# Kernel tuning notes

Hardware: AMD Instinct MI355X
Metric: run time of the kernel (lower is better)

The kernel has to match this reference:

```python
import jax, jax.numpy as jnp
import numpy as np

H = 12        # attention heads
BETA = 0.5    # blend weight between ctx-cosine probs and QK probs
LN_EPS = 1e-12


def layer_norm(x, g, b):
    mu = x.mean(-1, keepdims=True)
    var = ((x - mu) ** 2).mean(-1, keepdims=True)
    return (x - mu) * jax.lax.rsqrt(var + LN_EPS) * g + b


def setup_inputs() -> dict:
    key = jax.random.key(0)
    B, S, D, F, L = 16, 512, 768, 3072, 4
    ks = jax.random.split(key, 9)
    w = lambda k, shape: (jax.random.normal(k, shape, jnp.float32) * 0.02)
    return {
        "hidden_states": jax.random.normal(ks[0], (B, S, D), jnp.float32),
        "Wq": w(ks[1], (L, D, D)), "bq": jnp.zeros((L, D), jnp.float32),
        "Wk": w(ks[2], (L, D, D)), "bk": jnp.zeros((L, D), jnp.float32),
        "Wv": w(ks[3], (L, D, D)), "bv": jnp.zeros((L, D), jnp.float32),
        "Wc": w(ks[4], (L, D, D)), "bc": jnp.zeros((L, D), jnp.float32),
        "Wo": w(ks[5], (L, D, D)), "bo": jnp.zeros((L, D), jnp.float32),
        "g1": jnp.ones((L, D), jnp.float32), "b1": jnp.zeros((L, D), jnp.float32),
        "Wi": w(ks[6], (L, D, F)), "bi": jnp.zeros((L, F), jnp.float32),
        "Wo2": w(ks[7], (L, F, D)), "bo2": jnp.zeros((L, D), jnp.float32),
        "g2": jnp.ones((L, D), jnp.float32), "b2": jnp.zeros((L, D), jnp.float32),
    }


def reference(hidden_states, Wq, bq, Wk, bk, Wv, bv, Wc, bc, Wo, bo,
              g1, b1, Wi, bi, Wo2, bo2, g2, b2):
    B, S, D = hidden_states.shape
    Dh = D // H
    L = Wq.shape[0]
    eye = jnp.eye(S, dtype=hidden_states.dtype)
    scale = 1.0 / np.sqrt(Dh).astype(np.float32)

    def heads(t):  # [B,S,D] -> [B,H,S,Dh]
        return t.reshape(B, S, H, Dh).transpose(0, 2, 1, 3)

    x = hidden_states
    for i in range(L):  # small fixed layer loop
        q = heads(x @ Wq[i] + bq[i])
        k = heads(x @ Wk[i] + bk[i])
        v = heads(x @ Wv[i] + bv[i])
        c = heads(x @ Wc[i] + bc[i])

        # Branch 1: cosine-normalized context scores, flipped (1 - cos) + I
        cn = jnp.linalg.norm(c, axis=-1, keepdims=True)           # [B,H,S,1]
        denom = cn * jnp.swapaxes(cn, -1, -2)                     # [B,H,S,S]
        s1 = 1.0 - jnp.einsum('bhld,bhrd->bhlr', c, c) / denom + eye
        p1 = jax.nn.softmax(s1, axis=-1)

        # Branch 2: standard scaled QK scores
        s2 = jnp.einsum('bhld,bhrd->bhlr', q, k) * scale
        p2 = jax.nn.softmax(s2, axis=-1)

        p = BETA * p1 + (1.0 - BETA) * p2                          # beta blend
        ctx = jnp.einsum('bhlr,bhrd->bhld', p, v)                  # [B,H,S,Dh]
        ctx = ctx.transpose(0, 2, 1, 3).reshape(B, S, D)

        attn_out = layer_norm(ctx @ Wo[i] + bo[i] + x, g1[i], b1[i])
        h = jax.nn.gelu(attn_out @ Wi[i] + bi[i], approximate=False)
        x = layer_norm(h @ Wo2[i] + bo2[i] + attn_out, g2[i], b2[i])
    return x
```

## Files before the change

kernel.cpp:

```cpp
#include <hip/hip_runtime.h>
#include <math.h>

#define DD 768
#define FF 3072
#define SS 512
#define BB 16
#define NH 12
#define DH 64
#define NL 4
#define MM (BB*SS)

typedef __attribute__((ext_vector_type(8))) short short8;
typedef __attribute__((ext_vector_type(4))) float f32x4;

__device__ __forceinline__ unsigned short f2bf(float f) {
  unsigned u = __float_as_uint(f);
  return (unsigned short)((u + 0x7FFFu + ((u >> 16) & 1u)) >> 16);
}
__device__ __forceinline__ float bf2f(unsigned short s) {
  return __uint_as_float(((unsigned)s) << 16);
}

#define GLOAD_LDS(g, l) \
  __builtin_amdgcn_global_load_lds((const __attribute__((address_space(1))) void*)(g), \
                                   (__attribute__((address_space(3))) void*)(l), 16, 0, 0)

__global__ __launch_bounds__(256) void cvt_dual_k(const float* __restrict__ in,
                                                  float* __restrict__ outf,
                                                  unsigned short* __restrict__ outb, int n) {
  for (int i = blockIdx.x*256 + threadIdx.x; i < n; i += gridDim.x*256) {
    float v = in[i]; outf[i] = v; outb[i] = f2bf(v);
  }
}

__global__ __launch_bounds__(256) void tcvt_k(const float* __restrict__ src,
                                              unsigned short* __restrict__ dst,
                                              int K, int N) {
  __shared__ float t[32][33];
  const int n0 = blockIdx.x*32, k0 = blockIdx.y*32;
  const int tx = threadIdx.x & 31, ty = threadIdx.x >> 5;
#pragma unroll
  for (int i = 0; i < 32; i += 8)
    t[ty+i][tx] = src[(size_t)(k0+ty+i)*N + n0+tx];
  __syncthreads();
#pragma unroll
  for (int i = 0; i < 32; i += 8)
    dst[(size_t)(n0+ty+i)*K + k0+tx] = f2bf(t[tx][ty+i]);
}

__global__ __launch_bounds__(256) void bcat_k(const float* __restrict__ a,
                                              const float* __restrict__ b,
                                              const float* __restrict__ c,
                                              const float* __restrict__ d,
                                              float* __restrict__ out) {
  int i = blockIdx.x*256 + threadIdx.x;
  int w = i / 768;
  const float* s = (w == 0) ? a : (w == 1) ? b : (w == 2) ? c : d;
  out[i] = s[i - w*768];
}

template<int EPI, int OBF>
__global__ __launch_bounds__(256, 3) void mgemm_k(
    const unsigned short* __restrict__ A,
    const unsigned short* __restrict__ Bw,
    const float* __restrict__ bias,
    const float* __restrict__ resid,
    void* __restrict__ Cout, int M, int N, int K)
{
  __shared__ __align__(16) unsigned short As[2][128*32];
  __shared__ __align__(16) unsigned short Bs[2][128*32];
  const int nwg = gridDim.x * gridDim.y;
  int lin = blockIdx.y * gridDim.x + blockIdx.x;
  lin = (lin & 7) * (nwg >> 3) + (lin >> 3);
  const int bm = (lin / gridDim.x) * 128, bn = (lin % gridDim.x) * 128;
  const int tid = threadIdx.x;
  const int wave = tid >> 6, lane = tid & 63;
  const int wm = (wave >> 1)*64, wn = (wave & 1)*64;
  const int woff = wave*32*32;

  f32x4 acc[4][4] = {};

  const unsigned short* Ag = A  + (size_t)(bm + wave*32 + (lane>>2))*K + (lane&3)*8;
  const unsigned short* Bg = Bw + (size_t)(bn + wave*32 + (lane>>2))*K + (lane&3)*8;

  GLOAD_LDS(Ag,                As[0] + woff);
  GLOAD_LDS(Ag + 16*(size_t)K, As[0] + woff + 16*32);
  GLOAD_LDS(Bg,                Bs[0] + woff);
  GLOAD_LDS(Bg + 16*(size_t)K, Bs[0] + woff + 16*32);
  Ag += 32; Bg += 32;
  __syncthreads();

  const unsigned short* Ac = As[0]; unsigned short* An = As[1];
  const unsigned short* Bc = Bs[0]; unsigned short* Bn = Bs[1];
  const int nk = K >> 5;

#pragma unroll 1
  for (int t = 0; t < nk - 1; ++t) {
    GLOAD_LDS(Ag,                An + woff);
    GLOAD_LDS(Ag + 16*(size_t)K, An + woff + 16*32);
    GLOAD_LDS(Bg,                Bn + woff);
    GLOAD_LDS(Bg + 16*(size_t)K, Bn + woff + 16*32);
    Ag += 32; Bg += 32;

    short8 af[4], bfr[4];
#pragma unroll
    for (int i = 0; i < 4; ++i) {
      af[i]  = *(const short8*)&Ac[(wm + i*16 + (lane & 15))*32 + (lane >> 4)*8];
      bfr[i] = *(const short8*)&Bc[(wn + i*16 + (lane & 15))*32 + (lane >> 4)*8];
    }
    __builtin_amdgcn_s_setprio(1);
#pragma unroll
    for (int i = 0; i < 4; ++i)
#pragma unroll
      for (int j = 0; j < 4; ++j)
        acc[i][j] = __builtin_amdgcn_mfma_f32_16x16x32_bf16(af[i], bfr[j], acc[i][j], 0, 0, 0);
    __builtin_amdgcn_s_setprio(0);

    __syncthreads();
    const unsigned short* tA = Ac; Ac = An; An = (unsigned short*)tA;
    const unsigned short* tB = Bc; Bc = Bn; Bn = (unsigned short*)tB;
  }

  {
    short8 af[4], bfr[4];
#pragma unroll
    for (int i = 0; i < 4; ++i) {
      af[i]  = *(const short8*)&Ac[(wm + i*16 + (lane & 15))*32 + (lane >> 4)*8];
      bfr[i] = *(const short8*)&Bc[(wn + i*16 + (lane & 15))*32 + (lane >> 4)*8];
    }
#pragma unroll
    for (int i = 0; i < 4; ++i)
#pragma unroll
      for (int j = 0; j < 4; ++j)
        acc[i][j] = __builtin_amdgcn_mfma_f32_16x16x32_bf16(af[i], bfr[j], acc[i][j], 0, 0, 0);
  }

  const int col0 = bn + wn + (lane & 15);
  const int row0 = bm + wm + (lane >> 4)*4;
#pragma unroll
  for (int i = 0; i < 4; ++i) {
#pragma unroll
    for (int j = 0; j < 4; ++j) {
      const int n = col0 + j*16;
      const float bv = bias[n];
#pragma unroll
      for (int r = 0; r < 4; ++r) {
        const int m = row0 + i*16 + r;
        float v = acc[i][j][r] + bv;
        if (EPI == 1) v += resid[(size_t)m*N + n];
        if (EPI == 2) v = 0.5f*v*(1.0f + erff(v*0.70710678118654752f));
        if (OBF) ((unsigned short*)Cout)[(size_t)m*N + n] = f2bf(v);
        else     ((float*)Cout)[(size_t)m*N + n] = v;
      }
    }
  }
}

__global__ __launch_bounds__(256) void cnorm_k(const unsigned short* __restrict__ c,
                                               float* __restrict__ rn) {
  int idx = blockIdx.x*4 + (threadIdx.x >> 6);
  int lane = threadIdx.x & 63;
  int s  = idx % SS;
  int bh = idx / SS;
  int h  = bh % NH;
  int b  = bh / NH;
  float v = bf2f(c[((size_t)(b*SS + s))*FF + h*DH + lane]);
  float ss = v*v;
#pragma unroll
  for (int off = 32; off; off >>= 1) ss += __shfl_xor(ss, off, 64);
  if (lane == 0) rn[idx] = rsqrtf(ss);
}

__global__ __launch_bounds__(256) void vtrans_k(const unsigned short* __restrict__ v,
                                                unsigned short* __restrict__ VT) {
  __shared__ unsigned short t[64][72];
  const int s0 = blockIdx.x*64;
  const int h  = blockIdx.y;
  const int b  = blockIdx.z;
  const size_t base = (size_t)(b*SS)*FF + h*DH;
  const int row = threadIdx.x >> 2, seg = threadIdx.x & 3;
  const unsigned short* vg = v + base + (size_t)(s0+row)*FF + seg*16;
  *(uint4*)&t[row][seg*16]     = *(const uint4*)vg;
  *(uint4*)&t[row][seg*16 + 8] = *(const uint4*)(vg + 8);
  __syncthreads();
  unsigned short o[16];
#pragma unroll
  for (int u = 0; u < 16; ++u) o[u] = t[seg*16 + u][row];
  unsigned short* og = VT + ((size_t)(b*NH + h)*DH + row)*SS + s0 + seg*16;
  *(uint4*)og       = *(const uint4*)&o[0];
  *(uint4*)(og + 8) = *(const uint4*)&o[8];
}

__global__ __launch_bounds__(256, 3) void attn5_k(
    const unsigned short* __restrict__ q, const unsigned short* __restrict__ k,
    const unsigned short* __restrict__ c, const float* __restrict__ rn,
    const unsigned short* __restrict__ VT, unsigned short* __restrict__ ctxO)
{
  const int bid = blockIdx.x + 8*blockIdx.y + 96*blockIdx.z;
  const int l0  = ((bid >> 3) & 7) << 6;
  const int bh  = (bid & 7) + ((bid >> 6) << 3);
  const int h   = bh % NH;
  const int b   = bh / NH;
  const int tid = threadIdx.x;
  const int wave = tid >> 6, lane = tid & 63;
  const int wm = wave * 16;
  const int fr = lane & 15;
  const int fg = lane >> 4;
  const size_t base   = (size_t)(b*SS)*FF + h*DH;
  const size_t vtbase = (size_t)bh*DH*SS;

  __shared__ __align__(16) unsigned short Ks [2][64*72];
  __shared__ __align__(16) unsigned short Crs[2][64*72];
  __shared__ __align__(16) unsigned short Ps [4][16*72];
  unsigned short* Pw = Ps[wave];

  const unsigned short* qrow = q + base + (size_t)(l0 + wm + fr)*FF + fg*8;
  const unsigned short* crow = c + base + (size_t)(l0 + wm + fr)*FF + fg*8;
  const short8 aQ0 = *(const short8*)qrow;
  const short8 aQ1 = *(const short8*)(qrow + 32);
  const short8 aC0 = *(const short8*)crow;
  const short8 aC1 = *(const short8*)(crow + 32);

  float rnl[4];
#pragma unroll
  for (int reg = 0; reg < 4; ++reg)
    rnl[reg] = rn[(size_t)bh*SS + l0 + wm + fg*4 + reg];

  const int srow = tid >> 2, sseg = tid & 3;
  {
    const unsigned short* kg = k + base + (size_t)srow*FF + sseg*16;
    const unsigned short* cg = c + base + (size_t)srow*FF + sseg*16;
    *(uint4*)&Ks [0][srow*72 + sseg*16]     = *(const uint4*)kg;
    *(uint4*)&Ks [0][srow*72 + sseg*16 + 8] = *(const uint4*)(kg + 8);
    *(uint4*)&Crs[0][srow*72 + sseg*16]     = *(const uint4*)cg;
    *(uint4*)&Crs[0][srow*72 + sseg*16 + 8] = *(const uint4*)(cg + 8);
  }
  __syncthreads();

  float rs2[4], rs1[4];
#pragma unroll
  for (int r = 0; r < 4; ++r) { rs2[r] = 0.f; rs1[r] = 0.f; }
  f32x4 oc1[4] = {}, oc2[4] = {};

#pragma unroll 1
  for (int it = 0; it < 8; ++it) {
    const int r0 = it*64;
    const int cur = it & 1, nxt = cur ^ 1;

    uint4 nk0, nk1, nc0, nc1;
    if (it < 7) {
      const unsigned short* kg = k + base + (size_t)(r0 + 64 + srow)*FF + sseg*16;
      const unsigned short* cg = c + base + (size_t)(r0 + 64 + srow)*FF + sseg*16;
      nk0 = *(const uint4*)kg;  nk1 = *(const uint4*)(kg + 8);
      nc0 = *(const uint4*)cg;  nc1 = *(const uint4*)(cg + 8);
    }

    float rnr[4];
    short8 bv0[4], bv1[4];
#pragma unroll
    for (int nt = 0; nt < 4; ++nt) {
      rnr[nt] = rn[(size_t)bh*SS + r0 + nt*16 + fr];
      const unsigned short* vtr = VT + vtbase + (size_t)(nt*16 + fr)*SS + r0 + fg*8;
      bv0[nt] = *(const short8*)vtr;
      bv1[nt] = *(const short8*)(vtr + 32);
    }

    f32x4 s1a[4] = {}, s2a[4] = {};
#pragma unroll
    for (int nt = 0; nt < 4; ++nt) {
      const short8 bK0 = *(const short8*)&Ks [cur][(nt*16+fr)*72 + fg*8];
      const short8 bK1 = *(const short8*)&Ks [cur][(nt*16+fr)*72 + fg*8 + 32];
      const short8 bC0 = *(const short8*)&Crs[cur][(nt*16+fr)*72 + fg*8];
      const short8 bC1 = *(const short8*)&Crs[cur][(nt*16+fr)*72 + fg*8 + 32];
      s2a[nt] = __builtin_amdgcn_mfma_f32_16x16x32_bf16(aQ0, bK0, s2a[nt], 0,0,0);
      s2a[nt] = __builtin_amdgcn_mfma_f32_16x16x32_bf16(aQ1, bK1, s2a[nt], 0,0,0);
      s1a[nt] = __builtin_amdgcn_mfma_f32_16x16x32_bf16(aC0, bC0, s1a[nt], 0,0,0);
      s1a[nt] = __builtin_amdgcn_mfma_f32_16x16x32_bf16(aC1, bC1, s1a[nt], 0,0,0);
    }

    float sv1[4][4], sv2[4][4];
#pragma unroll
    for (int nt = 0; nt < 4; ++nt)
#pragma unroll
      for (int reg = 0; reg < 4; ++reg) {
        const int ql = wm + fg*4 + reg;
        const int rr = nt*16 + fr;
        sv2[reg][nt] = s2a[nt][reg] * 0.125f;
        sv1[reg][nt] = 1.0f - s1a[nt][reg]*rnl[reg]*rnr[nt]
                     + ((l0+ql) == (r0+rr) ? 1.0f : 0.0f);
      }

#pragma unroll
    for (int reg = 0; reg < 4; ++reg) {
      const int prow = (fg*4 + reg)*72;
#pragma unroll
      for (int nt = 0; nt < 4; ++nt) {
        const float x1 = __expf(sv1[reg][nt] - 3.0f);
        Pw[prow + nt*16 + fr] = f2bf(x1);
        rs1[reg] += x1;
      }
    }
    {
      const short8 p0 = *(const short8*)&Pw[fr*72 + fg*8];
      const short8 p1 = *(const short8*)&Pw[fr*72 + fg*8 + 32];
#pragma unroll
      for (int nt = 0; nt < 4; ++nt) {
        oc1[nt] = __builtin_amdgcn_mfma_f32_16x16x32_bf16(p0, bv0[nt], oc1[nt], 0,0,0);
        oc1[nt] = __builtin_amdgcn_mfma_f32_16x16x32_bf16(p1, bv1[nt], oc1[nt], 0,0,0);
      }
    }

#pragma unroll
    for (int reg = 0; reg < 4; ++reg) {
      const int prow = (fg*4 + reg)*72;
#pragma unroll
      for (int nt = 0; nt < 4; ++nt) {
        const float x2 = __expf(sv2[reg][nt] - 3.0f);
        Pw[prow + nt*16 + fr] = f2bf(x2);
        rs2[reg] += x2;
      }
    }
    {
      const short8 p0 = *(const short8*)&Pw[fr*72 + fg*8];
      const short8 p1 = *(const short8*)&Pw[fr*72 + fg*8 + 32];
#pragma unroll
      for (int nt = 0; nt < 4; ++nt) {
        oc2[nt] = __builtin_amdgcn_mfma_f32_16x16x32_bf16(p0, bv0[nt], oc2[nt], 0,0,0);
        oc2[nt] = __builtin_amdgcn_mfma_f32_16x16x32_bf16(p1, bv1[nt], oc2[nt], 0,0,0);
      }
    }

    if (it < 7) {
      *(uint4*)&Ks [nxt][srow*72 + sseg*16]     = nk0;
      *(uint4*)&Ks [nxt][srow*72 + sseg*16 + 8] = nk1;
      *(uint4*)&Crs[nxt][srow*72 + sseg*16]     = nc0;
      *(uint4*)&Crs[nxt][srow*72 + sseg*16 + 8] = nc1;
    }
    __syncthreads();
  }

#pragma unroll
  for (int reg = 0; reg < 4; ++reg) {
    float t1 = rs1[reg], t2 = rs2[reg];
#pragma unroll
    for (int off = 1; off < 16; off <<= 1) {
      t1 += __shfl_xor(t1, off, 64);
      t2 += __shfl_xor(t2, off, 64);
    }
    const float i1 = 0.5f / t1;
    const float i2 = 0.5f / t2;
    const int prow = (fg*4 + reg)*72;
#pragma unroll
    for (int nt = 0; nt < 4; ++nt)
      Pw[prow + nt*16 + fr] = f2bf(oc1[nt][reg]*i1 + oc2[nt][reg]*i2);
  }
  {
    const int row = lane >> 2, seg = lane & 3;
    const int Mrow = b*SS + l0 + wm + row;
    unsigned short* og = ctxO + (size_t)Mrow*DD + h*DH + seg*16;
    *(uint4*)og       = *(const uint4*)&Pw[row*72 + seg*16];
    *(uint4*)(og + 8) = *(const uint4*)&Pw[row*72 + seg*16 + 8];
  }
}

__global__ __launch_bounds__(256) void ln_k(const float* __restrict__ in,
                                            const float* __restrict__ g,
                                            const float* __restrict__ b,
                                            float* __restrict__ outf,
                                            unsigned short* __restrict__ outb) {
  __shared__ float xs[DD];
  __shared__ float red[4];
  const int tid = threadIdx.x;
  const float* xr = in + (size_t)blockIdx.x * DD;
  float* xo = outf + (size_t)blockIdx.x * DD;
  unsigned short* xbr = outb + (size_t)blockIdx.x * DD;
  float s = 0.f;
  for (int d = tid; d < DD; d += 256) { float v = xr[d]; xs[d] = v; s += v; }
#pragma unroll
  for (int off = 32; off; off >>= 1) s += __shfl_xor(s, off, 64);
  if ((tid & 63) == 0) red[tid >> 6] = s;
  __syncthreads();
  float mu = (red[0]+red[1]+red[2]+red[3]) * (1.f/DD);
  __syncthreads();
  float s2 = 0.f;
  for (int d = tid; d < DD; d += 256) { float t = xs[d]-mu; s2 += t*t; }
#pragma unroll
  for (int off = 32; off; off >>= 1) s2 += __shfl_xor(s2, off, 64);
  if ((tid & 63) == 0) red[tid >> 6] = s2;
  __syncthreads();
  float var = (red[0]+red[1]+red[2]+red[3]) * (1.f/DD);
  float rstd = rsqrtf(var + 1e-12f);
  for (int d = tid; d < DD; d += 256) {
    float o = (xs[d]-mu)*rstd*g[d] + b[d];
    xo[d] = o;
    xbr[d] = f2bf(o);
  }
}

extern "C" void kernel_launch(void* const* d_in, const int* in_sizes, int n_in,
                              void* d_out, int out_size, void* d_ws, size_t ws_size,
                              hipStream_t stream) {
  const float* hs  = (const float*)d_in[0];
  const float* Wq  = (const float*)d_in[1];  const float* bq  = (const float*)d_in[2];
  const float* Wk  = (const float*)d_in[3];  const float* bk  = (const float*)d_in[4];
  const float* Wv  = (const float*)d_in[5];  const float* bv  = (const float*)d_in[6];
  const float* Wc  = (const float*)d_in[7];  const float* bc  = (const float*)d_in[8];
  const float* Wo  = (const float*)d_in[9];  const float* bo  = (const float*)d_in[10];
  const float* g1  = (const float*)d_in[11]; const float* b1  = (const float*)d_in[12];
  const float* Wi  = (const float*)d_in[13]; const float* bi  = (const float*)d_in[14];
  const float* Wo2 = (const float*)d_in[15]; const float* bo2 = (const float*)d_in[16];
  const float* g2  = (const float*)d_in[17]; const float* b2  = (const float*)d_in[18];

  const size_t XN  = (size_t)MM * DD;
  const size_t HN  = (size_t)MM * FF;
  const int    nBH = BB*NH*SS;
  const size_t WTN = 7667712;

  char* p = (char*)d_ws;
  float*          x      = (float*)p;           p += XN*4;
  float*          attnf  = (float*)p;           p += XN*4;
  unsigned short* qkvc16 = (unsigned short*)p;  p += HN*2;
  unsigned short* xb16   = (unsigned short*)p;  p += XN*2;
  unsigned short* ctx16  = (unsigned short*)p;  p += XN*2;
  unsigned short* attn16 = (unsigned short*)p;  p += XN*2;
  unsigned short* vt16   = (unsigned short*)p;  p += XN*2;
  unsigned short* WT     = (unsigned short*)p;  p += WTN*2;
  float*          bqkvc  = (float*)p;           p += 3072*4;
  float*          cnb    = (float*)p;           p += (size_t)nBH*4;
  const size_t need = (size_t)(p - (char*)d_ws);
  if (ws_size < need) return;

  unsigned short* WqkvcT = WT;
  unsigned short* WoT    = WT + 2359296;
  unsigned short* WiT    = WT + 2949120;
  unsigned short* Wo2T   = WT + 5308416;
  unsigned short* hb16   = qkvc16;

  cvt_dual_k<<<4096, 256, 0, stream>>>(hs, x, xb16, (int)XN);

  dim3 gGQ(FF/128, MM/128);
  dim3 gGD(DD/128, MM/128);
  dim3 gA(SS/64, NH, BB);
  dim3 tDD(DD/32, DD/32);
  dim3 tDF(FF/32, DD/32);
  dim3 tFD(DD/32, FF/32);

  for (int i = 0; i < NL; ++i) {
    const size_t wD = (size_t)i*DD*DD, wF = (size_t)i*DD*FF;
    tcvt_k<<<tDD, 256, 0, stream>>>(Wq + wD, WqkvcT,            DD, DD);
    tcvt_k<<<tDD, 256, 0, stream>>>(Wk + wD, WqkvcT +  768*768, DD, DD);
    tcvt_k<<<tDD, 256, 0, stream>>>(Wv + wD, WqkvcT + 1536*768, DD, DD);
    tcvt_k<<<tDD, 256, 0, stream>>>(Wc + wD, WqkvcT + 2304*768, DD, DD);
    tcvt_k<<<tDD, 256, 0, stream>>>(Wo + wD, WoT,  DD, DD);
    tcvt_k<<<tDF, 256, 0, stream>>>(Wi + wF, WiT,  DD, FF);
    tcvt_k<<<tFD, 256, 0, stream>>>(Wo2 + wF, Wo2T, FF, DD);
    bcat_k<<<12, 256, 0, stream>>>(bq + (size_t)i*DD, bk + (size_t)i*DD,
                                   bv + (size_t)i*DD, bc + (size_t)i*DD, bqkvc);

    mgemm_k<0,1><<<gGQ, 256, 0, stream>>>(xb16, WqkvcT, bqkvc, nullptr, qkvc16, MM, FF, DD);

    cnorm_k<<<nBH/4, 256, 0, stream>>>(qkvc16 + 2304, cnb);
    vtrans_k<<<gA, 256, 0, stream>>>(qkvc16 + 1536, vt16);
    attn5_k<<<gA, 256, 0, stream>>>(qkvc16, qkvc16 + 768, qkvc16 + 2304,
                                    cnb, vt16, ctx16);

    mgemm_k<1,0><<<gGD, 256, 0, stream>>>(ctx16, WoT, bo + (size_t)i*DD, x, attnf, MM, DD, DD);
    ln_k<<<MM, 256, 0, stream>>>(attnf, g1 + (size_t)i*DD, b1 + (size_t)i*DD, attnf, attn16);

    mgemm_k<2,1><<<gGQ, 256, 0, stream>>>(attn16, WiT, bi + (size_t)i*FF, nullptr, hb16, MM, FF, DD);
    mgemm_k<1,0><<<gGD, 256, 0, stream>>>(hb16, Wo2T, bo2 + (size_t)i*DD, attnf, x, MM, DD, FF);
    float* lnout = (i == NL-1) ? (float*)d_out : x;
    ln_k<<<MM, 256, 0, stream>>>(x, g2 + (size_t)i*DD, b2 + (size_t)i*DD, lnout, xb16);
  }
}
```

Before: 1.474 ms.

## Add 256x256 tile GEMM kernel for QKVC and FFN-up projections

Adds a new 512-thread GEMM kernel with 256x256 output tiles, double-buffered LDS filled by direct global-to-LDS loads, XOR-swizzled reads, an interleaved load/MFMA schedule with priority hints, and a grid remap for locality. It replaces the 128x128 GEMM for the two N=3072 projections (fused QKVC and the GELU up-projection). The larger tiles raise operand reuse and cut global traffic, and the staged schedule overlaps loads with matrix math. In exchange it uses much more LDS and many more accumulator registers per block, and it launches only 384 workgroups, which may leave some compute units underused or unevenly loaded.

Measured after the change: 1.565 ms. 6.2% more time.

```diff
diff --git a/kernel.cpp b/kernel.cpp
--- a/kernel.cpp
+++ b/kernel.cpp
@@ -156,6 +156,143 @@
   }
 }
 
+template<int EPI>
+__global__ __launch_bounds__(512, 2) void mg256_k(
+    const unsigned short* __restrict__ A,
+    const unsigned short* __restrict__ Bw,
+    const float* __restrict__ bias,
+    unsigned short* __restrict__ Cout, int M, int N, int K)
+{
+  __shared__ __align__(16) unsigned short Ab[2][256*64];
+  __shared__ __align__(16) unsigned short Bb[2][256*64];
+  const int nwg = gridDim.x * gridDim.y;
+  int lin = blockIdx.y * gridDim.x + blockIdx.x;
+  lin = (lin & 7) * (nwg >> 3) + (lin >> 3);
+  const int bm = (lin / gridDim.x) * 256, bn = (lin % gridDim.x) * 256;
+  const int tid = threadIdx.x;
+  const int wave = tid >> 6, lane = tid & 63;
+  const int wr = wave >> 2, wc = wave & 3;
+  const int fr = lane & 15, fg = lane >> 4;
+  const int xsw = (fr & 8) ? 4 : 0;
+
+  f32x4 acc[8][4] = {};
+  short8 bfrag[4][2];
+
+  const int srow = tid >> 3;
+  const int sseg = (tid & 7) ^ ((wave & 1) << 2);
+  const unsigned short* Asrc = A  + (size_t)(bm + srow)*K + sseg*8;
+  const unsigned short* Bsrc = Bw + (size_t)(bn + srow)*K + sseg*8;
+  const int ldst = wave * 512;
+
+#define MG_STGA(q, bf, kk) GLOAD_LDS(Asrc + (size_t)((q)*64)*K + (kk), &Ab[bf][(q)*4096 + ldst])
+#define MG_STGB(q, bf, kk) GLOAD_LDS(Bsrc + (size_t)((q)*64)*K + (kk), &Bb[bf][(q)*4096 + ldst])
+
+  const int arow0 = wr*128 + fr;
+  const int brow0 = wc*64 + fr;
+#define MG_A(m, s) (*(const short8*)&Ac[(arow0 + (m)*16)*64 + ((((s)*4) + fg) ^ xsw)*8])
+#define MG_B(n, s) (*(const short8*)&Bc[(brow0 + (n)*16)*64 + ((((s)*4) + fg) ^ xsw)*8])
+
+#define MG_MFMA(m0, a00, a01, a10, a11) do { \
+    __builtin_amdgcn_s_setprio(1); \
+    _Pragma("unroll") \
+    for (int n = 0; n < 4; ++n) { \
+      acc[m0][n]   = __builtin_amdgcn_mfma_f32_16x16x32_bf16(a00, bfrag[n][0], acc[m0][n],   0,0,0); \
+      acc[m0][n]   = __builtin_amdgcn_mfma_f32_16x16x32_bf16(a01, bfrag[n][1], acc[m0][n],   0,0,0); \
+      acc[m0+1][n] = __builtin_amdgcn_mfma_f32_16x16x32_bf16(a10, bfrag[n][0], acc[m0+1][n], 0,0,0); \
+      acc[m0+1][n] = __builtin_amdgcn_mfma_f32_16x16x32_bf16(a11, bfrag[n][1], acc[m0+1][n], 0,0,0); \
+    } \
+    __builtin_amdgcn_s_setprio(0); } while (0)
+
+  const int nk = K >> 6;
+
+  MG_STGB(0, 0, 0); MG_STGB(1, 0, 0); MG_STGB(2, 0, 0); MG_STGB(3, 0, 0);
+  MG_STGA(0, 0, 0); MG_STGA(2, 0, 0); MG_STGA(1, 0, 0); MG_STGA(3, 0, 0);
+  asm volatile("s_waitcnt vmcnt(2)" ::: "memory");
+  __builtin_amdgcn_sched_barrier(0);
+  __builtin_amdgcn_s_barrier();
+
+  int cur = 0;
+#pragma unroll 1
+  for (int t = 0; t < nk - 1; ++t) {
+    const int nx = cur ^ 1;
+    const int kk = (t + 1) << 6;
+    const unsigned short* Ac = Ab[cur];
+    const unsigned short* Bc = Bb[cur];
+    short8 x0, x1, y0, y1;
+    x0 = MG_A(0,0); x1 = MG_A(0,1); y0 = MG_A(1,0); y1 = MG_A(1,1);
+#pragma unroll
+    for (int n = 0; n < 4; ++n) { bfrag[n][0] = MG_B(n,0); bfrag[n][1] = MG_B(n,1); }
+    MG_STGB(0, nx, kk); MG_STGB(1, nx, kk);
+    __builtin_amdgcn_s_barrier();
+    MG_MFMA(0, x0, x1, y0, y1);
+    __builtin_amdgcn_s_barrier();
+    x0 = MG_A(2,0); x1 = MG_A(2,1); y0 = MG_A(3,0); y1 = MG_A(3,1);
+    MG_STGB(2, nx, kk); MG_STGB(3, nx, kk);
+    __builtin_amdgcn_s_barrier();
+    MG_MFMA(2, x0, x1, y0, y1);
+    asm volatile("s_waitcnt vmcnt(4)" ::: "memory");
+    __builtin_amdgcn_sched_barrier(0);
+    __builtin_amdgcn_s_barrier();
+    x0 = MG_A(4,0); x1 = MG_A(4,1); y0 = MG_A(5,0); y1 = MG_A(5,1);
+    MG_STGA(0, nx, kk); MG_STGA(2, nx, kk);
+    __builtin_amdgcn_s_barrier();
+    MG_MFMA(4, x0, x1, y0, y1);
+    __builtin_amdgcn_s_barrier();
+    x0 = MG_A(6,0); x1 = MG_A(6,1); y0 = MG_A(7,0); y1 = MG_A(7,1);
+    MG_STGA(1, nx, kk); MG_STGA(3, nx, kk);
+    __builtin_amdgcn_s_barrier();
+    MG_MFMA(6, x0, x1, y0, y1);
+    asm volatile("s_waitcnt vmcnt(2)" ::: "memory");
+    __builtin_amdgcn_sched_barrier(0);
+    __builtin_amdgcn_s_barrier();
+    cur = nx;
+  }
+  {
+    const unsigned short* Ac = Ab[cur];
+    const unsigned short* Bc = Bb[cur];
+    short8 x0, x1, y0, y1;
+    x0 = MG_A(0,0); x1 = MG_A(0,1); y0 = MG_A(1,0); y1 = MG_A(1,1);
+#pragma unroll
+    for (int n = 0; n < 4; ++n) { bfrag[n][0] = MG_B(n,0); bfrag[n][1] = MG_B(n,1); }
+    __builtin_amdgcn_s_barrier();
+    MG_MFMA(0, x0, x1, y0, y1);
+    __builtin_amdgcn_s_barrier();
+    x0 = MG_A(2,0); x1 = MG_A(2,1); y0 = MG_A(3,0); y1 = MG_A(3,1);
+    __builtin_amdgcn_s_barrier();
+    MG_MFMA(2, x0, x1, y0, y1);
+    asm volatile("s_waitcnt vmcnt(0)" ::: "memory");
+    __builtin_amdgcn_sched_barrier(0);
+    __builtin_amdgcn_s_barrier();
+    x0 = MG_A(4,0); x1 = MG_A(4,1); y0 = MG_A(5,0); y1 = MG_A(5,1);
+    __builtin_amdgcn_s_barrier();
+    MG_MFMA(4, x0, x1, y0, y1);
+    __builtin_amdgcn_s_barrier();
+    x0 = MG_A(6,0); x1 = MG_A(6,1); y0 = MG_A(7,0); y1 = MG_A(7,1);
+    MG_MFMA(6, x0, x1, y0, y1);
+  }
+#undef MG_STGA
+#undef MG_STGB
+#undef MG_A
+#undef MG_B
+#undef MG_MFMA
+
+  const int crow0 = bm + wr*128 + fg*4;
+  const int ccol0 = bn + wc*64 + fr;
+#pragma unroll
+  for (int n = 0; n < 4; ++n) {
+    const float bv = bias[ccol0 + n*16];
+#pragma unroll
+    for (int m = 0; m < 8; ++m) {
+#pragma unroll
+      for (int r = 0; r < 4; ++r) {
+        float v = acc[m][n][r] + bv;
+        if (EPI == 2) v = 0.5f*v*(1.0f + erff(v*0.70710678118654752f));
+        Cout[(size_t)(crow0 + m*16 + r)*N + ccol0 + n*16] = f2bf(v);
+      }
+    }
+  }
+}
+
 __global__ __launch_bounds__(256) void cnorm_k(const unsigned short* __restrict__ c,
                                                float* __restrict__ rn) {
   int idx = blockIdx.x*4 + (threadIdx.x >> 6);
@@ -438,7 +575,7 @@
 
   cvt_dual_k<<<4096, 256, 0, stream>>>(hs, x, xb16, (int)XN);
 
-  dim3 gGQ(FF/128, MM/128);
+  dim3 gG2(FF/256, MM/256);
   dim3 gGD(DD/128, MM/128);
   dim3 gA(SS/64, NH, BB);
   dim3 tDD(DD/32, DD/32);
@@ -457,7 +594,7 @@
     bcat_k<<<12, 256, 0, stream>>>(bq + (size_t)i*DD, bk + (size_t)i*DD,
                                    bv + (size_t)i*DD, bc + (size_t)i*DD, bqkvc);
 
-    mgemm_k<0,1><<<gGQ, 256, 0, stream>>>(xb16, WqkvcT, bqkvc, nullptr, qkvc16, MM, FF, DD);
+    mg256_k<0><<<gG2, 512, 0, stream>>>(xb16, WqkvcT, bqkvc, qkvc16, MM, FF, DD);
 
     cnorm_k<<<nBH/4, 256, 0, stream>>>(qkvc16 + 2304, cnb);
     vtrans_k<<<gA, 256, 0, stream>>>(qkvc16 + 1536, vt16);
@@ -467,7 +604,7 @@
     mgemm_k<1,0><<<gGD, 256, 0, stream>>>(ctx16, WoT, bo + (size_t)i*DD, x, attnf, MM, DD, DD);
     ln_k<<<MM, 256, 0, stream>>>(attnf, g1 + (size_t)i*DD, b1 + (size_t)i*DD, attnf, attn16);
 
-    mgemm_k<2,1><<<gGQ, 256, 0, stream>>>(attn16, WiT, bi + (size_t)i*FF, nullptr, hb16, MM, FF, DD);
+    mg256_k<2><<<gG2, 512, 0, stream>>>(attn16, WiT, bi + (size_t)i*FF, hb16, MM, FF, DD);
     mgemm_k<1,0><<<gGD, 256, 0, stream>>>(hb16, Wo2T, bo2 + (size_t)i*DD, attnf, x, MM, DD, FF);
     float* lnout = (i == NL-1) ? (float*)d_out : x;
     ln_k<<<MM, 256, 0, stream>>>(x, g2 + (size_t)i*DD, b2 + (size_t)i*DD, lnout, xb16);
```
